# Kernel optimization log

Hardware: AMD Instinct MI355X
Metric: run time of the kernel (lower is better)

Reference implementation:

```python
import jax, jax.numpy as jnp
import numpy as np

B, S, T, H, E = 64, 256, 128, 1024, 512


def setup_inputs() -> dict:
    key = jax.random.key(0)
    ks = jax.random.split(key, 16)
    sc = 0.02
    inp = {
        "trg_embed": jax.random.normal(ks[0], (B, T, E), jnp.float32),
        "encoder_hidden": jax.random.normal(ks[1], (B, S, 2 * H), jnp.float32),
        "encoder_final": jax.random.normal(ks[2], (1, B, 2 * H), jnp.float32),
        "src_mask": jnp.ones((B, 1, S), dtype=bool),
        "trg_mask": jnp.ones((B, 1, T), dtype=bool),
        # bridge: Linear(2H -> H, bias)
        "W_bridge": jax.random.normal(ks[3], (H, 2 * H), jnp.float32) * sc,
        "b_bridge": jnp.zeros((H,), jnp.float32),
        # Bahdanau attention: key/query/energy layers (no bias)
        "W_key": jax.random.normal(ks[4], (H, 2 * H), jnp.float32) * sc,
        "W_query": jax.random.normal(ks[5], (H, H), jnp.float32) * sc,
        "v_energy": jax.random.normal(ks[6], (H,), jnp.float32) * sc,
        # GRU (1 layer): input size E + 2H, hidden H. PyTorch gate order [r, z, n].
        "W_ih": jax.random.normal(ks[7], (3 * H, E + 2 * H), jnp.float32) * sc,
        "W_hh": jax.random.normal(ks[8], (3 * H, H), jnp.float32) * sc,
        "b_ih": jnp.zeros((3 * H,), jnp.float32),
        "b_hh": jnp.zeros((3 * H,), jnp.float32),
        # pre_output: Linear(H + 2H + E -> H, no bias)
        "W_pre": jax.random.normal(ks[9], (H, H + 2 * H + E), jnp.float32) * sc,
    }
    return inp


def reference(trg_embed, encoder_hidden, encoder_final, src_mask, trg_mask,
              W_bridge, b_bridge, W_key, W_query, v_energy,
              W_ih, W_hh, b_ih, b_hh, W_pre):
    neg_inf = jnp.float32(-1e9)
    # init_hidden: tanh(bridge(encoder_final)) -> [num_layers, B, H]; take last layer
    h0 = jnp.tanh(jnp.einsum('lbk,hk->lbh', encoder_final, W_bridge) + b_bridge)[-1]  # [B, H]
    # precompute projected keys once (as in forward())
    proj_key = jnp.einsum('bsk,hk->bsh', encoder_hidden, W_key)  # [B, S, H]
    mask = src_mask[:, 0, :]  # [B, S]

    def step(h, prev_embed):  # h: [B,H], prev_embed: [B,E]
        # Bahdanau attention with query = last-layer hidden state
        q = h @ W_query.T                                        # [B, H]
        energies = jnp.tanh(q[:, None, :] + proj_key) @ v_energy  # [B, S]
        energies = jnp.where(mask, energies, neg_inf)
        alphas = jax.nn.softmax(energies, axis=-1)               # [B, S]
        context = jnp.einsum('bs,bsd->bd', alphas, encoder_hidden)  # [B, 2H]
        # GRU step on concat(prev_embed, context)
        x = jnp.concatenate([prev_embed, context], axis=-1)      # [B, E+2H]
        gi = x @ W_ih.T + b_ih                                   # [B, 3H]
        gh = h @ W_hh.T + b_hh                                   # [B, 3H]
        i_r, i_z, i_n = jnp.split(gi, 3, axis=-1)
        h_r, h_z, h_n = jnp.split(gh, 3, axis=-1)
        r = jax.nn.sigmoid(i_r + h_r)
        z = jax.nn.sigmoid(i_z + h_z)
        n = jnp.tanh(i_n + r * h_n)
        h_new = (1.0 - z) * n + z * h                            # [B, H]
        # pre-output projection (dropout disabled: eval / p effectively identity)
        pre = jnp.concatenate([prev_embed, h_new, context], axis=-1) @ W_pre.T  # [B, H]
        return h_new, (h_new, pre)

    h_final, (states, pres) = jax.lax.scan(step, h0, jnp.swapaxes(trg_embed, 0, 1))
    decoder_states = jnp.swapaxes(states, 0, 1)      # [B, T, H]
    pre_output_vectors = jnp.swapaxes(pres, 0, 1)    # [B, T, H]
    hidden = h_final[None]                            # [num_layers=1, B, H]
    return decoder_states, hidden, pre_output_vectors
```

## Files before the change

kernel.cpp:

```cpp
#include <hip/hip_runtime.h>

#define Bn 64
#define Sn 256
#define Tn 128
#define Hn 1024
#define En 512
#define H2n 2048
#define NBLK 256
#define NTHR 1024

#define WCTX 10
#define WH 12

#define GW 0
#define PWc 0
#define PWh 32768
#define PWq 49152
#define PWe 65536
#define PREP 73728
#define SCR2 75776
#define SCR 147456
#define GIL 155648
#define LDS_BYTES 161792

typedef __attribute__((ext_vector_type(8))) short short8v;
typedef __attribute__((ext_vector_type(4))) float floatx4;

__device__ __forceinline__ unsigned short f2bf(float f) {
  union { float f; unsigned u; } x; x.f = f;
  unsigned r = x.u + 0x7fffu + ((x.u >> 16) & 1u);
  return (unsigned short)(r >> 16);
}
__device__ __forceinline__ float bf2f(unsigned short u) {
  union { unsigned u; float f; } x; x.u = ((unsigned)u) << 16; return x.f;
}
__device__ __forceinline__ float sigm(float x) { return 1.f / (1.f + __expf(-x)); }
__device__ __forceinline__ float tanh_f(float x) {
  float e = __expf(2.f * x);
  return 1.f - 2.f / (e + 1.f);
}
__device__ __forceinline__ short8v ldf(const unsigned short* p) { return *(const short8v*)p; }
#define MFMA(a, b, c) __builtin_amdgcn_mfma_f32_16x16x32_bf16(a, b, c, 0, 0, 0)

__device__ __forceinline__ float ldc_f(const float* p) {
  return __hip_atomic_load(p, __ATOMIC_RELAXED, __HIP_MEMORY_SCOPE_AGENT);
}
__device__ __forceinline__ void stc_f(float* p, float v) {
  __hip_atomic_store(p, v, __ATOMIC_RELAXED, __HIP_MEMORY_SCOPE_AGENT);
}
__device__ __forceinline__ void stc_u32(unsigned* p, unsigned v) {
  __hip_atomic_store(p, v, __ATOMIC_RELAXED, __HIP_MEMORY_SCOPE_AGENT);
}
__device__ __forceinline__ unsigned long long ldc_u64(const unsigned long long* p) {
  return __hip_atomic_load(p, __ATOMIC_RELAXED, __HIP_MEMORY_SCOPE_AGENT);
}
__device__ __forceinline__ void stc_u64(unsigned long long* p, unsigned long long v) {
  __hip_atomic_store(p, v, __ATOMIC_RELAXED, __HIP_MEMORY_SCOPE_AGENT);
}

__device__ __forceinline__ void bar_lds() {
  __builtin_amdgcn_sched_barrier(0);
  asm volatile("s_waitcnt lgkmcnt(0)" ::: "memory");
  __builtin_amdgcn_s_barrier();
  __builtin_amdgcn_sched_barrier(0);
}

__device__ __forceinline__ short8v packf(const float* p) {
  float4 e0 = *(const float4*)p, e1 = *(const float4*)(p + 4);
  short8v x;
  x[0] = (short)f2bf(e0.x); x[1] = (short)f2bf(e0.y);
  x[2] = (short)f2bf(e0.z); x[3] = (short)f2bf(e0.w);
  x[4] = (short)f2bf(e1.x); x[5] = (short)f2bf(e1.y);
  x[6] = (short)f2bf(e1.z); x[7] = (short)f2bf(e1.w);
  return x;
}

__global__ __launch_bounds__(256) void cast_kernel(const float4* __restrict__ src,
                                                   uint2* __restrict__ dst, int n4) {
  for (int i = blockIdx.x * blockDim.x + threadIdx.x; i < n4; i += gridDim.x * blockDim.x) {
    float4 v = src[i];
    uint2 p;
    p.x = (unsigned)f2bf(v.x) | ((unsigned)f2bf(v.y) << 16);
    p.y = (unsigned)f2bf(v.z) | ((unsigned)f2bf(v.w) << 16);
    dst[i] = p;
  }
}

__global__ __launch_bounds__(256) void bridge_kernel(const float* __restrict__ ef,
                                                     const float* __restrict__ Wb,
                                                     const float* __restrict__ bb,
                                                     float* __restrict__ h0out,
                                                     unsigned short* __restrict__ hb0) {
  __shared__ float efs[H2n];
  const int b = blockIdx.x >> 2, jq = blockIdx.x & 3;
  const int j = jq * 256 + threadIdx.x;
  for (int i = threadIdx.x; i < H2n; i += 256) efs[i] = ef[(size_t)b * H2n + i];
  __syncthreads();
  const float* wr = Wb + (size_t)j * H2n;
  float acc = bb[j];
  for (int k = 0; k < H2n; k += 4) {
    float4 wv = *(const float4*)&wr[k];
    acc += efs[k] * wv.x + efs[k + 1] * wv.y + efs[k + 2] * wv.z + efs[k + 3] * wv.w;
  }
  float th = tanhf(acc);
  h0out[(size_t)b * Hn + j] = th;
  hb0[(size_t)b * Hn + j] = f2bf(th);
}

__global__ __launch_bounds__(256) void pk_gemm(const unsigned short* __restrict__ A,
                                               const unsigned short* __restrict__ Bw,
                                               unsigned short* __restrict__ pk) {
  const int bid = blockIdx.x;
  const int mt = bid >> 4, nt = bid & 15;
  const int w = threadIdx.x >> 6, lane = threadIdx.x & 63;
  const int lm = lane & 15, lk = lane >> 4, ko = lk * 8;
  const unsigned short* arow = A + (size_t)(mt * 64 + w * 16 + lm) * 2048 + ko;
  const unsigned short* b0 = Bw + (size_t)(nt * 64 + lm) * 2048 + ko;
  const unsigned short* b1 = Bw + (size_t)(nt * 64 + 16 + lm) * 2048 + ko;
  const unsigned short* b2 = Bw + (size_t)(nt * 64 + 32 + lm) * 2048 + ko;
  const unsigned short* b3 = Bw + (size_t)(nt * 64 + 48 + lm) * 2048 + ko;
  floatx4 c0 = {0,0,0,0}, c1 = {0,0,0,0}, c2 = {0,0,0,0}, c3 = {0,0,0,0};
  for (int k = 0; k < 2048; k += 32) {
    short8v a = ldf(arow + k);
    c0 = MFMA(a, ldf(b0 + k), c0);
    c1 = MFMA(a, ldf(b1 + k), c1);
    c2 = MFMA(a, ldf(b2 + k), c2);
    c3 = MFMA(a, ldf(b3 + k), c3);
  }
  const int m = mt * 64 + w * 16 + lk * 4;
  const int j = nt * 64 + lm;
#pragma unroll
  for (int r = 0; r < 4; ++r) {
    unsigned short* row = pk + (size_t)(m + r) * 1024 + j;
    row[0]  = f2bf(c0[r]);
    row[16] = f2bf(c1[r]);
    row[32] = f2bf(c2[r]);
    row[48] = f2bf(c3[r]);
  }
}

struct DA {
  const float* emb; const float* v; const float* bih; const float* bhh;
  const unsigned short* pk; const unsigned short* ehb;
  const unsigned short* Wih; const unsigned short* Whh;
  const unsigned short* Wpre; const unsigned short* Wq;
  float* hbuf; unsigned short* hbR; float* qbuf; float* wbuf; float* psump;
  unsigned short* ctxR; unsigned* bar; float* out;
};

__device__ __forceinline__ void gbar(unsigned* bar, int tid, unsigned idx, int inv) {
  asm volatile("s_waitcnt vmcnt(0)" ::: "memory");
  __syncthreads();
  if (tid == 0) {
    unsigned old = __hip_atomic_fetch_add(bar, 1u, __ATOMIC_RELAXED, __HIP_MEMORY_SCOPE_AGENT);
    if (old + 1u == (unsigned)NBLK * idx) {
      __hip_atomic_store(bar + 32, idx, __ATOMIC_RELAXED, __HIP_MEMORY_SCOPE_AGENT);
    } else {
      unsigned g;
      do {
        __builtin_amdgcn_s_sleep(2);
        g = __hip_atomic_load(bar + 32, __ATOMIC_RELAXED, __HIP_MEMORY_SCOPE_AGENT);
      } while (g < idx);
    }
  }
  __syncthreads();
  if (inv) __builtin_amdgcn_fence(__ATOMIC_ACQUIRE, "agent");
}

__device__ __forceinline__ void gbar_pk(const DA& a, unsigned* bar, int tid, unsigned idx,
                                        int inv, int b, int sc4, int w, int lane,
                                        short8v* pkr) {
  asm volatile("s_waitcnt vmcnt(0)" ::: "memory");
  __syncthreads();
  __builtin_amdgcn_sched_barrier(0);
#pragma unroll
  for (int i = 0; i < 4; ++i) {
    const unsigned short* prow =
        a.pk + ((size_t)b * Sn + sc4 * 64 + w * 4 + i) * Hn + lane * 16;
    pkr[i] = ldf(prow);
    pkr[4 + i] = ldf(prow + 8);
  }
  __builtin_amdgcn_sched_barrier(0);
  if (tid == 0) {
    unsigned old = __hip_atomic_fetch_add(bar, 1u, __ATOMIC_RELAXED, __HIP_MEMORY_SCOPE_AGENT);
    if (old + 1u == (unsigned)NBLK * idx) {
      __hip_atomic_store(bar + 32, idx, __ATOMIC_RELAXED, __HIP_MEMORY_SCOPE_AGENT);
    } else {
      unsigned g;
      do {
        __builtin_amdgcn_s_sleep(2);
        g = __hip_atomic_load(bar + 32, __ATOMIC_RELAXED, __HIP_MEMORY_SCOPE_AGENT);
      } while (g < idx);
    }
  }
  __syncthreads();
  if (inv) __builtin_amdgcn_fence(__ATOMIC_ACQUIRE, "agent");
}

__device__ __forceinline__ void phA(const DA& a, char* dsm, int bid, int tid,
                                    int w, int lane, int t, const short8v* pkr) {
  const int b = bid >> 2, sc4 = bid & 3;
  float* w_s = (float*)(dsm + SCR);
  float* q_s = (float*)(dsm + SCR + 1024);
  if (tid < 256) {
    const unsigned long long* qp = (const unsigned long long*)(a.qbuf + (size_t)b * Hn) + tid * 2;
    unsigned long long u0 = ldc_u64(qp), u1 = ldc_u64(qp + 1);
    union { unsigned long long u; float f[2]; } x0, x1; x0.u = u0; x1.u = u1;
    q_s[tid * 4] = x0.f[0]; q_s[tid * 4 + 1] = x0.f[1];
    q_s[tid * 4 + 2] = x1.f[0]; q_s[tid * 4 + 3] = x1.f[1];
  }
  __syncthreads();
  float qr[16], vr[16];
  const float* vp = a.v + lane * 16;
#pragma unroll
  for (int i = 0; i < 16; i += 4) {
    *(float4*)&qr[i] = *(const float4*)&q_s[lane * 16 + i];
    *(float4*)&vr[i] = *(const float4*)(vp + i);
  }
#pragma unroll
  for (int i = 0; i < 4; ++i) {
    float ep = 0.f;
#pragma unroll
    for (int e = 0; e < 8; ++e) {
      ep += vr[e] * tanh_f(qr[e] + bf2f((unsigned short)pkr[i][e]));
      ep += vr[8 + e] * tanh_f(qr[8 + e] + bf2f((unsigned short)pkr[4 + i][e]));
    }
#pragma unroll
    for (int m = 1; m < 64; m <<= 1) ep += __shfl_xor(ep, m, 64);
    if (lane == 0) {
      float wv = __expf(ep - 20.f);
      w_s[w * 4 + i] = wv;
      stc_f(a.wbuf + (size_t)b * Sn + sc4 * 64 + w * 4 + i, wv);
    }
  }
  const int ls = lane >> 2, ldcx = lane & 3;
  const int dchunk = w * 4 + ldcx;
  const unsigned short* ebase = a.ehb + (size_t)b * Sn * H2n + sc4 * 512 + dchunk * 8;
  short8v er[8];
#pragma unroll
  for (int k = 0; k < 8; ++k) er[k] = ldf(ebase + (size_t)(ls + k * 16) * H2n);
  bar_lds();
  if (tid < 64) {
    float wv = w_s[tid];
#pragma unroll
    for (int m = 1; m < 64; m <<= 1) wv += __shfl_xor(wv, m, 64);
    if (tid == 0) stc_f(a.psump + sc4 * 64 + b, wv);
  }
  asm volatile("s_waitcnt vmcnt(0)" ::: "memory");
  __syncthreads();
  if (tid == 0) stc_u32(&a.bar[64 + (b << 2) + sc4], (unsigned)(t + 1));
  if (tid < 4) {
    while (__hip_atomic_load(&a.bar[64 + (b << 2) + tid], __ATOMIC_RELAXED,
                             __HIP_MEMORY_SCOPE_AGENT) < (unsigned)(t + 1))
      __builtin_amdgcn_s_sleep(1);
  }
  __syncthreads();
  float* wn = (float*)(dsm + SCR);
  float psinv = 1.f / (ldc_f(a.psump + b) + ldc_f(a.psump + 64 + b) +
                       ldc_f(a.psump + 128 + b) + ldc_f(a.psump + 192 + b));
  if (tid < 256) wn[tid] = ldc_f(a.wbuf + (size_t)b * Sn + tid) * psinv;
  __syncthreads();
  float acc[8] = {};
#pragma unroll
  for (int k = 0; k < 8; ++k) {
    float wf = wn[ls + k * 16];
#pragma unroll
    for (int e2 = 0; e2 < 8; ++e2) acc[e2] += wf * bf2f((unsigned short)er[k][e2]);
  }
#pragma unroll
  for (int k = 8; k < 16; ++k) {
    short8v e = ldf(ebase + (size_t)(ls + k * 16) * H2n);
    float wf = wn[ls + k * 16];
#pragma unroll
    for (int e2 = 0; e2 < 8; ++e2) acc[e2] += wf * bf2f((unsigned short)e[e2]);
  }
#pragma unroll
  for (int m = 4; m < 64; m <<= 1) {
#pragma unroll
    for (int e2 = 0; e2 < 8; ++e2) acc[e2] += __shfl_xor(acc[e2], m, 64);
  }
  if (ls == 0) {
    union { unsigned long long u[2]; unsigned short s[8]; } p;
#pragma unroll
    for (int e2 = 0; e2 < 8; ++e2) p.s[e2] = f2bf(acc[e2]);
    unsigned long long* dst = (unsigned long long*)(
        a.ctxR + (size_t)(t % WCTX) * Bn * H2n + (size_t)b * H2n + sc4 * 512 + dchunk * 8);
    stc_u64(dst, p.u[0]); stc_u64(dst + 1, p.u[1]);
  }
}

__device__ __forceinline__ void gate_c(const DA& a, char* dsm, int j0, int w,
                                       int lane, int tid, int t, int cur, int nxt) {
  float* scr = (float*)(dsm + SCR);
  for (int i = tid; i < 2048; i += NTHR) scr[i] = 0.f;
  __syncthreads();
  const int mt = w & 3, ks = w >> 2;
  const int lm = lane & 15, lk = lane >> 4;
  const int arow = mt * 16 + lm, jb = lm & 7;
  const unsigned short* ctxrow =
      a.ctxR + (size_t)(t % WCTX) * Bn * H2n + (size_t)arow * H2n + lk * 8;
  const unsigned short* hrow =
      a.hbR + (size_t)(t % WH) * Bn * Hn + (size_t)arow * Hn + lk * 8;
  const char* wb0 = dsm + GW + (size_t)((0 * 8 + jb) * 384) * 16;
  const char* wb1 = dsm + GW + (size_t)((1 * 8 + jb) * 384) * 16;
  const char* wb2 = dsm + GW + (size_t)((2 * 8 + jb) * 384) * 16;
  floatx4 ar = {0,0,0,0}, az = {0,0,0,0}, ain = {0,0,0,0}, ahn = {0,0,0,0};
#pragma unroll 4
  for (int kc = ks * 24; kc < ks * 24 + 24; ++kc) {
    short8v x = (kc < 64) ? ldf(ctxrow + kc * 32) : ldf(hrow + (kc - 64) * 32);
    const size_t slot = (size_t)((kc * 4 + lk) ^ jb) * 16;
    ar = MFMA(x, *(const short8v*)(wb0 + slot), ar);
    az = MFMA(x, *(const short8v*)(wb1 + slot), az);
    if (kc < 64) ain = MFMA(x, *(const short8v*)(wb2 + slot), ain);
    else         ahn = MFMA(x, *(const short8v*)(wb2 + slot), ahn);
  }
  if (lm < 8) {
#pragma unroll
    for (int r = 0; r < 4; ++r) {
      const int bb = mt * 16 + lk * 4 + r;
      atomicAdd(&scr[(0 * 64 + bb) * 8 + jb], ar[r]);
      atomicAdd(&scr[(1 * 64 + bb) * 8 + jb], az[r]);
      atomicAdd(&scr[(2 * 64 + bb) * 8 + jb], ain[r]);
      atomicAdd(&scr[(3 * 64 + bb) * 8 + jb], ahn[r]);
    }
  }
  __syncthreads();
  if (tid < 256) {
    const int bb = tid >> 2, jj = (tid & 3) * 2;
    float* gil = (float*)(dsm + GIL);
    float hn2[2];
#pragma unroll
    for (int u = 0; u < 2; ++u) {
      const int j = jj + u, jg = j0 + j;
      float grv = scr[(0 * 64 + bb) * 8 + j] + gil[(0 * 64 + bb) * 8 + j] + a.bhh[jg];
      float gzv = scr[(1 * 64 + bb) * 8 + j] + gil[(1 * 64 + bb) * 8 + j] + a.bhh[Hn + jg];
      float ginv = scr[(2 * 64 + bb) * 8 + j] + gil[(2 * 64 + bb) * 8 + j];
      float ghnv = scr[(3 * 64 + bb) * 8 + j] + a.bhh[2 * Hn + jg];
      float rr = sigm(grv), zz = sigm(gzv);
      float nn = tanh_f(ginv + rr * ghnv);
      float hold = a.hbuf[(size_t)cur * Bn * Hn + (size_t)bb * Hn + jg];
      float hnew = (1.f - zz) * nn + zz * hold;
      hn2[u] = hnew;
      a.hbuf[(size_t)nxt * Bn * Hn + (size_t)bb * Hn + jg] = hnew;
      a.out[((size_t)bb * Tn + t) * Hn + jg] = hnew;
      if (t == Tn - 1) a.out[(size_t)Bn * Tn * Hn + (size_t)bb * Hn + jg] = hnew;
    }
    unsigned hpack = (unsigned)f2bf(hn2[0]) | ((unsigned)f2bf(hn2[1]) << 16);
    stc_u32((unsigned*)(a.hbR + (size_t)((t + 1) % WH) * Bn * Hn +
                        (size_t)bb * Hn + j0 + jj), hpack);
  }
}

__device__ __forceinline__ void pre_c(const DA& a, char* dsm, int j0, int w,
                                      int lane, int tid, int t) {
  float* prep = (float*)(dsm + PREP);
  for (int i = tid; i < 512; i += NTHR) prep[i] = 0.f;
  __syncthreads();
  const int mt = w & 3, ks = w >> 2;
  const int lm = lane & 15, lk = lane >> 4;
  const int arow = mt * 16 + lm, jb = lm & 7;
  const unsigned short* ctxrow =
      a.ctxR + (size_t)(t % WCTX) * Bn * H2n + (size_t)arow * H2n + lk * 8;
  const float* ep = a.emb + ((size_t)arow * Tn + t) * En + lk * 8;
  const char* we = dsm + PWe + (size_t)(jb * 64) * 16;
  const char* wc = dsm + PWc + (size_t)(jb * 256) * 16;
  floatx4 acc = {0,0,0,0};
#pragma unroll 4
  for (int kc = ks * 20; kc < ks * 20 + 20; ++kc) {
    if (kc < 16) {
      acc = MFMA(packf(ep + kc * 32),
                 *(const short8v*)(we + (size_t)((kc * 4 + lk) ^ jb) * 16), acc);
    } else {
      const int c = kc - 16;
      acc = MFMA(ldf(ctxrow + c * 32),
                 *(const short8v*)(wc + (size_t)((c * 4 + lk) ^ jb) * 16), acc);
    }
  }
  if (lm < 8) {
#pragma unroll
    for (int r = 0; r < 4; ++r)
      atomicAdd(&prep[(mt * 16 + lk * 4 + r) * 8 + jb], acc[r]);
  }
  __syncthreads();
}

__device__ __forceinline__ void pre_d(const DA& a, char* dsm, int j0, int w,
                                      int lane, int tid, int t, int hslot, int doPre) {
  float* scr = (float*)(dsm + SCR2);
  for (int i = tid; i < 1024; i += NTHR) scr[i] = 0.f;
  __syncthreads();
  const int mt = w & 3, part = w >> 2;
  const int lm = lane & 15, lk = lane >> 4;
  const int arow = mt * 16 + lm, jb = lm & 7;
  const unsigned short* hrow =
      a.hbR + (size_t)hslot * Bn * Hn + (size_t)arow * Hn + lk * 8;
  const int isQ = part >> 1;
  const char* wbase = dsm + (isQ ? PWq : PWh) + (size_t)(jb * 128) * 16;
  if (doPre || isQ) {
    floatx4 acc = {0,0,0,0};
    const int k0 = (part & 1) * 16;
#pragma unroll 4
    for (int kh = k0; kh < k0 + 16; ++kh)
      acc = MFMA(ldf(hrow + kh * 32),
                 *(const short8v*)(wbase + (size_t)((kh * 4 + lk) ^ jb) * 16), acc);
    if (lm < 8) {
#pragma unroll
      for (int r = 0; r < 4; ++r)
        atomicAdd(&scr[(isQ * 64 + mt * 16 + lk * 4 + r) * 8 + jb], acc[r]);
    }
  }
  __syncthreads();
  if (tid < 256) {
    const int bb = tid >> 2, jj = (tid & 3) * 2;
    float* prep = (float*)(dsm + PREP);
#pragma unroll
    for (int u = 0; u < 2; ++u) {
      const int j = jj + u, jg = j0 + j;
      if (doPre) {
        float pv = scr[(0 * 64 + bb) * 8 + j] + prep[bb * 8 + j];
        a.out[(size_t)Bn * Tn * Hn + (size_t)Bn * Hn + ((size_t)bb * Tn + t) * Hn + jg] = pv;
      }
      stc_f(a.qbuf + (size_t)bb * Hn + jg, scr[(1 * 64 + bb) * 8 + j]);
    }
  }
}

__device__ __forceinline__ void gi_compute(const DA& a, char* dsm, int j0, int w,
                                           int lane, int t1) {
  const int mt = w & 3, g = w >> 2;
  if (g >= 3) return;
  const int lm = lane & 15, lk = lane >> 4;
  const int arow = mt * 16 + lm;
  const unsigned short* wrow = a.Wih + (size_t)(g * Hn + j0 + (lm & 7)) * 2560 + lk * 8;
  const float* ep = a.emb + ((size_t)arow * Tn + t1) * En + lk * 8;
  floatx4 acc = {0,0,0,0};
#pragma unroll 4
  for (int kk = 0; kk < 16; ++kk)
    acc = MFMA(packf(ep + kk * 32), ldf(wrow + kk * 32), acc);
  if (lm < 8) {
    float* gil = (float*)(dsm + GIL);
    float bv = a.bih[g * Hn + j0 + lm];
#pragma unroll
    for (int r = 0; r < 4; ++r)
      gil[(g * 64 + mt * 16 + lk * 4 + r) * 8 + lm] = acc[r] + bv;
  }
}

__global__ void __attribute__((amdgpu_flat_work_group_size(1024, 1024),
                               amdgpu_waves_per_eu(4, 4)))
dec_kernel(DA a) {
  extern __shared__ char dsm[];
  const int tid = threadIdx.x, bid = blockIdx.x;
  const int w = tid >> 6, lane = tid & 63;
  const bool isGate = bid < 128;
  const int j0 = (isGate ? bid : bid - 128) * 8;
  const int pb = bid >> 2, psc4 = bid & 3;

  if (isGate) {
    for (int idx = tid; idx < 9216; idx += NTHR) {
      int row = idx / 384, c = idx % 384;
      int g = row >> 3, j = row & 7;
      const unsigned short* src = (c < 256)
          ? a.Wih + (size_t)(g * Hn + j0 + j) * 2560 + 512 + c * 8
          : a.Whh + (size_t)(g * Hn + j0 + j) * Hn + (c - 256) * 8;
      *(uint4*)(dsm + (size_t)(row * 384 + (c ^ j)) * 16) = *(const uint4*)src;
    }
  } else {
    for (int idx = tid; idx < 4608; idx += NTHR) {
      const unsigned short* src; size_t dst;
      if (idx < 2048) {
        int j = idx >> 8, c = idx & 255;
        src = a.Wpre + (size_t)(j0 + j) * 3584 + 1536 + c * 8;
        dst = PWc + (size_t)(j * 256 + (c ^ j)) * 16;
      } else if (idx < 3072) {
        int i = idx - 2048, j = i >> 7, c = i & 127;
        src = a.Wpre + (size_t)(j0 + j) * 3584 + 512 + c * 8;
        dst = PWh + (size_t)(j * 128 + (c ^ j)) * 16;
      } else if (idx < 4096) {
        int i = idx - 3072, j = i >> 7, c = i & 127;
        src = a.Wq + (size_t)(j0 + j) * Hn + c * 8;
        dst = PWq + (size_t)(j * 128 + (c ^ j)) * 16;
      } else {
        int i = idx - 4096, j = i >> 6, c = i & 63;
        src = a.Wpre + (size_t)(j0 + j) * 3584 + c * 8;
        dst = PWe + (size_t)(j * 64 + (c ^ j)) * 16;
      }
      *(uint4*)(dsm + dst) = *(const uint4*)src;
    }
  }
  __syncthreads();

  short8v pkr[8];
  unsigned bi = 1;
  if (isGate) gi_compute(a, dsm, j0, w, lane, 0);
  else pre_d(a, dsm, j0, w, lane, tid, 0, 0, 0);
  gbar_pk(a, a.bar, tid, bi++, 0, pb, psc4, w, lane, pkr);

  for (int t = 0; t < Tn; ++t) {
    const int cur = t & 1, nxt = cur ^ 1;
    phA(a, dsm, bid, tid, w, lane, t, pkr);
    gbar(a.bar, tid, bi++, 0);
    if (isGate) gate_c(a, dsm, j0, w, lane, tid, t, cur, nxt);
    else pre_c(a, dsm, j0, w, lane, tid, t);
    gbar(a.bar, tid, bi++, 0);
    if (isGate) { if (t + 1 < Tn) gi_compute(a, dsm, j0, w, lane, t + 1); }
    else pre_d(a, dsm, j0, w, lane, tid, t, (t + 1) % WH, 1);
    gbar_pk(a, a.bar, tid, bi++, (t & 7) == 7, pb, psc4, w, lane, pkr);
  }
}

extern "C" void kernel_launch(void* const* d_in, const int* in_sizes, int n_in,
                              void* d_out, int out_size, void* d_ws, size_t ws_size,
                              hipStream_t stream) {
  (void)in_sizes; (void)n_in; (void)out_size; (void)ws_size;
  const float* emb = (const float*)d_in[0];
  const float* eh  = (const float*)d_in[1];
  const float* ef  = (const float*)d_in[2];
  const float* Wb  = (const float*)d_in[5];
  const float* bb  = (const float*)d_in[6];
  const float* Wk  = (const float*)d_in[7];
  const float* Wq  = (const float*)d_in[8];
  const float* v   = (const float*)d_in[9];
  const float* Wih = (const float*)d_in[10];
  const float* Whh = (const float*)d_in[11];
  const float* bih = (const float*)d_in[12];
  const float* bhh = (const float*)d_in[13];
  const float* Wpre= (const float*)d_in[14];
  float* out = (float*)d_out;

  char* wsb = (char*)d_ws;
  unsigned short* ehb  = (unsigned short*)(wsb + 0);
  unsigned short* pkb  = (unsigned short*)(wsb + 67108864);
  unsigned short* Wihb = (unsigned short*)(wsb + 100663296);
  unsigned short* Whhb = (unsigned short*)(wsb + 116391936);
  unsigned short* Wpreb= (unsigned short*)(wsb + 122683392);
  unsigned short* Wqb  = (unsigned short*)(wsb + 130023424);
  unsigned short* Wkb  = (unsigned short*)(wsb + 132120576);
  unsigned short* ctxR = (unsigned short*)(wsb + 132120576);
  unsigned short* hbR  = (unsigned short*)(wsb + 134742016);
  float* hbuf = (float*)(wsb + 136314880);
  float* qbuf = (float*)(wsb + 137101312);
  float* wbuf = (float*)(wsb + 137363456);
  float* psump= (float*)(wsb + 137428992);
  unsigned* bar = (unsigned*)(wsb + 137695232);

  hipMemsetAsync(bar, 0, 4096, stream);
  cast_kernel<<<2048, 256, 0, stream>>>((const float4*)eh, (uint2*)ehb, Bn * Sn * H2n / 4);
  cast_kernel<<<2048, 256, 0, stream>>>((const float4*)Wih, (uint2*)Wihb, 3 * Hn * 2560 / 4);
  cast_kernel<<<1024, 256, 0, stream>>>((const float4*)Whh, (uint2*)Whhb, 3 * Hn * Hn / 4);
  cast_kernel<<<1024, 256, 0, stream>>>((const float4*)Wpre, (uint2*)Wpreb, Hn * 3584 / 4);
  cast_kernel<<<512, 256, 0, stream>>>((const float4*)Wq, (uint2*)Wqb, Hn * Hn / 4);
  cast_kernel<<<512, 256, 0, stream>>>((const float4*)Wk, (uint2*)Wkb, Hn * H2n / 4);
  pk_gemm<<<4096, 256, 0, stream>>>(ehb, Wkb, pkb);
  bridge_kernel<<<256, 256, 0, stream>>>(ef, Wb, bb, hbuf, hbR);

  DA da;
  da.emb = emb; da.v = v; da.bih = bih; da.bhh = bhh;
  da.pk = pkb; da.ehb = ehb;
  da.Wih = Wihb; da.Whh = Whhb; da.Wpre = Wpreb; da.Wq = Wqb;
  da.hbuf = hbuf; da.hbR = hbR; da.qbuf = qbuf; da.wbuf = wbuf; da.psump = psump;
  da.ctxR = ctxR; da.bar = bar; da.out = out;

  hipFuncSetAttribute(reinterpret_cast<const void*>(&dec_kernel),
                      hipFuncAttributeMaxDynamicSharedMemorySize, LDS_BYTES);
  void* kp[] = { (void*)&da };
  hipLaunchCooperativeKernel(reinterpret_cast<const void*>(&dec_kernel),
                             dim3(NBLK), dim3(NTHR), kp, LDS_BYTES, stream);
}
```

Measured before the change: 11.18 ms.

## Replace two grid-wide barriers per step with targeted producer-consumer counters

In the persistent decoder loop, the full grid barrier after gate_c/pre_c and the one after gi_compute/pre_d are replaced by one-directional counter signals. Gate blocks bump a counter after gate_c, and only pre blocks wait on it before pre_d. Pre blocks bump a second counter after pre_d, and every block waits on it before the next step, still prefetching projected keys while it waits. This aims to cut global barrier latency and let gate blocks start the next gi_compute early, at the cost of subtler memory-ordering reasoning: fences and acquire happen only every 8 steps.

```diff
diff --git a/kernel.cpp b/kernel.cpp
--- a/kernel.cpp
+++ b/kernel.cpp
@@ -192,6 +192,50 @@
         g = __hip_atomic_load(bar + 32, __ATOMIC_RELAXED, __HIP_MEMORY_SCOPE_AGENT);
       } while (g < idx);
     }
+  }
+  __syncthreads();
+  if (inv) __builtin_amdgcn_fence(__ATOMIC_ACQUIRE, "agent");
+}
+
+__device__ __forceinline__ void gateC_signal(unsigned* bar, int tid) {
+  asm volatile("s_waitcnt vmcnt(0)" ::: "memory");
+  __syncthreads();
+  if (tid == 0)
+    __hip_atomic_fetch_add(bar + 512, 1u, __ATOMIC_RELAXED, __HIP_MEMORY_SCOPE_AGENT);
+}
+__device__ __forceinline__ void gateC_wait(unsigned* bar, int tid, unsigned tgt) {
+  __syncthreads();
+  if (tid == 0) {
+    while (__hip_atomic_load(bar + 512, __ATOMIC_RELAXED, __HIP_MEMORY_SCOPE_AGENT) < tgt)
+      __builtin_amdgcn_s_sleep(1);
+  }
+  __syncthreads();
+}
+
+__device__ __forceinline__ void preD_wait_pk(const DA& a, unsigned* bar, int tid,
+                                             unsigned tgt, int inv, int isGate,
+                                             int b, int sc4, int w, int lane,
+                                             short8v* pkr) {
+  if (!isGate) {
+    asm volatile("s_waitcnt vmcnt(0)" ::: "memory");
+    __syncthreads();
+    if (tid == 0)
+      __hip_atomic_fetch_add(bar + 544, 1u, __ATOMIC_RELAXED, __HIP_MEMORY_SCOPE_AGENT);
+  } else {
+    __syncthreads();
+  }
+  __builtin_amdgcn_sched_barrier(0);
+#pragma unroll
+  for (int i = 0; i < 4; ++i) {
+    const unsigned short* prow =
+        a.pk + ((size_t)b * Sn + sc4 * 64 + w * 4 + i) * Hn + lane * 16;
+    pkr[i] = ldf(prow);
+    pkr[4 + i] = ldf(prow + 8);
+  }
+  __builtin_amdgcn_sched_barrier(0);
+  if (tid == 0) {
+    while (__hip_atomic_load(bar + 544, __ATOMIC_RELAXED, __HIP_MEMORY_SCOPE_AGENT) < tgt)
+      __builtin_amdgcn_s_sleep(1);
   }
   __syncthreads();
   if (inv) __builtin_amdgcn_fence(__ATOMIC_ACQUIRE, "agent");
@@ -500,12 +544,17 @@
     const int cur = t & 1, nxt = cur ^ 1;
     phA(a, dsm, bid, tid, w, lane, t, pkr);
     gbar(a.bar, tid, bi++, 0);
-    if (isGate) gate_c(a, dsm, j0, w, lane, tid, t, cur, nxt);
-    else pre_c(a, dsm, j0, w, lane, tid, t);
-    gbar(a.bar, tid, bi++, 0);
-    if (isGate) { if (t + 1 < Tn) gi_compute(a, dsm, j0, w, lane, t + 1); }
-    else pre_d(a, dsm, j0, w, lane, tid, t, (t + 1) % WH, 1);
-    gbar_pk(a, a.bar, tid, bi++, (t & 7) == 7, pb, psc4, w, lane, pkr);
+    if (isGate) {
+      gate_c(a, dsm, j0, w, lane, tid, t, cur, nxt);
+      gateC_signal(a.bar, tid);
+      if (t + 1 < Tn) gi_compute(a, dsm, j0, w, lane, t + 1);
+    } else {
+      pre_c(a, dsm, j0, w, lane, tid, t);
+      gateC_wait(a.bar, tid, 128u * (unsigned)(t + 1));
+      pre_d(a, dsm, j0, w, lane, tid, t, (t + 1) % WH, 1);
+    }
+    preD_wait_pk(a, a.bar, tid, 128u * (unsigned)(t + 1), (t & 7) == 7,
+                 isGate, pb, psc4, w, lane, pkr);
   }
 }
 
```

Result: no change. 10.97 ms (-1.8%).
